# Kernel tuning notes

Measured on AMD Instinct MI355X. Metric: run time of the kernel, lower is better.

The kernel has to match this reference:

```python
import jax, jax.numpy as jnp
import numpy as np

NUM_HEADS = 16


def _rope(x_BHLd, freqs_cis):
    # x: [B,H,L,d], freqs_cis: [L, d//2, 2] (cos, sin)
    B, H, L, d = x_BHLd.shape
    xs = x_BHLd.reshape(B, H, L, d // 2, 2)
    fc = freqs_cis.reshape(1, 1, L, d // 2, 2)
    real = xs[..., 0] * fc[..., 0] - xs[..., 1] * fc[..., 1]
    imag = xs[..., 1] * fc[..., 0] + xs[..., 0] * fc[..., 1]
    return jnp.stack([real, imag], axis=-1).reshape(B, H, L, d)


def setup_inputs() -> dict:
    key = jax.random.key(0)
    k1, k2 = jax.random.split(key)
    B, L, D = 1, 4096, 1024
    d = D // NUM_HEADS
    x = jax.random.normal(k1, (B, L, D), dtype=jnp.float32)
    Wqkv = jax.random.normal(k2, (D, 3 * D), dtype=jnp.float32) * (D ** -0.5)
    bqkv = jnp.zeros((3 * D,), dtype=jnp.float32)
    # true rotary cos/sin table: [L, d//2, 2]
    base = 10000.0
    inv_freq = 1.0 / (base ** (jnp.arange(0, d, 2, dtype=jnp.float32) / d))  # [d//2]
    t = jnp.arange(L, dtype=jnp.float32)
    ang = jnp.outer(t, inv_freq)  # [L, d//2]
    freqs_cis = jnp.stack([jnp.cos(ang), jnp.sin(ang)], axis=-1)  # [L, d//2, 2]
    return {"x": x, "freqs_cis": freqs_cis, "Wqkv": Wqkv, "bqkv": bqkv}


def reference(x, freqs_cis, Wqkv, bqkv):
    B, L, D = x.shape
    H = NUM_HEADS
    d = D // H
    qkv = x @ Wqkv + bqkv  # [B,L,3D]
    q, k, v = jnp.split(qkv, 3, axis=-1)
    split = lambda t: t.reshape(B, L, H, d).transpose(0, 2, 1, 3)  # [B,H,L,d]
    q, k, v = split(q), split(k), split(v)
    q = _rope(q, freqs_cis)
    k = _rope(k, freqs_cis)
    scale = 1.0 / jnp.sqrt(jnp.asarray(d, dtype=q.dtype))
    scores = jnp.einsum('bhqd,bhkd->bhqk', q, k) * scale  # [B,H,L,L]
    causal = jnp.tril(jnp.ones((L, L), dtype=bool))
    scores = jnp.where(causal, scores, jnp.asarray(-jnp.inf, dtype=scores.dtype))
    probs = jax.nn.softmax(scores, axis=-1)
    out = jnp.einsum('bhqk,bhkd->bhqd', probs, v)  # [B,H,L,d]
    return out.transpose(0, 2, 1, 3).reshape(B, L, D)
```

## Files before the change

### kernel.cpp

```cpp
#include <hip/hip_runtime.h>

typedef short short8 __attribute__((ext_vector_type(8)));
typedef float f32x4 __attribute__((ext_vector_type(4)));
typedef unsigned short u16;
typedef unsigned short u16x4 __attribute__((ext_vector_type(4)));
typedef unsigned short u16x8 __attribute__((ext_vector_type(8)));

#define L_SEQ 4096
#define NHEAD 16
#define HDIM  64
#define DMODEL 1024
#define N3    3072
#define HL    (L_SEQ * HDIM)

__device__ __forceinline__ u16 f2bf(float f) {
  union { float f; unsigned u; } v; v.f = f;
  return (u16)((v.u + 0x7fffu + ((v.u >> 16) & 1u)) >> 16);
}

__device__ __forceinline__ unsigned cvt_pk_bf16(float lo, float hi) {
  unsigned r;
  asm("v_cvt_pk_bf16_f32 %0, %1, %2" : "=v"(r) : "v"(lo), "v"(hi));
  return r;
}

__device__ __forceinline__ void gl2lds16(const void* g, void* l) {
  __builtin_amdgcn_global_load_lds(
      (const __attribute__((address_space(1))) unsigned int*)g,
      (__attribute__((address_space(3))) unsigned int*)l, 16, 0, 0);
}

__device__ __forceinline__ float fexp2(float x) { return __builtin_amdgcn_exp2f(x); }

__global__ void cvt_fused_kernel(const float* __restrict__ x, u16* __restrict__ xb,
                                 const float* __restrict__ W, u16* __restrict__ Wt) {
  if (blockIdx.x < 2048) {
    int i = blockIdx.x * blockDim.x + threadIdx.x;
    const f32x4* p = (const f32x4*)x + (size_t)i * 2;
    f32x4 a = p[0], b = p[1];
    u16x8 o;
    o[0] = f2bf(a[0]); o[1] = f2bf(a[1]); o[2] = f2bf(a[2]); o[3] = f2bf(a[3]);
    o[4] = f2bf(b[0]); o[5] = f2bf(b[1]); o[6] = f2bf(b[2]); o[7] = f2bf(b[3]);
    ((u16x8*)xb)[i] = o;
  } else {
    __shared__ float t[64][65];
    int idx = blockIdx.x - 2048;
    int k0 = (idx & 15) * 64, n0 = (idx >> 4) * 64;
    int tr = threadIdx.x >> 4;
    int tc = (threadIdx.x & 15) * 4;
    for (int rr = tr; rr < 64; rr += 16) {
      f32x4 v = *(const f32x4*)&W[(size_t)(k0 + rr) * N3 + n0 + tc];
      t[rr][tc] = v[0]; t[rr][tc + 1] = v[1]; t[rr][tc + 2] = v[2]; t[rr][tc + 3] = v[3];
    }
    __syncthreads();
    for (int rr = tr; rr < 64; rr += 16) {
      u16x4 o;
      o[0] = f2bf(t[tc + 0][rr]); o[1] = f2bf(t[tc + 1][rr]);
      o[2] = f2bf(t[tc + 2][rr]); o[3] = f2bf(t[tc + 3][rr]);
      *(u16x4*)&Wt[(size_t)(n0 + rr) * DMODEL + k0 + tc] = o;
    }
  }
}

#define GBM 128
#define GBN 128
#define GBK 64

__global__ __launch_bounds__(256, 2) void gemm_qkv_kernel(
    const u16* __restrict__ xb, const u16* __restrict__ wt,
    const float* __restrict__ bias, const float* __restrict__ freqs,
    u16* __restrict__ Qb, u16* __restrict__ Kb, u16* __restrict__ Vt) {
  __shared__ u16 Asm[GBM * GBK];
  __shared__ u16 Bsm[GBN * GBK];
  const int tid = threadIdx.x, lane = tid & 63, wid = tid >> 6;
  const int lr = lane & 15, lh = lane >> 4;
  const int swz = (blockIdx.x % 8) * 96 + blockIdx.x / 8;
  const int bx = swz % (N3 / GBN), by = swz / (N3 / GBN);
  const int m0 = by * GBM, n0 = bx * GBN;
  const int wr = wid >> 1, wc = wid & 1;
  const char* xbB = (const char*)xb;
  const char* wtB = (const char*)wt;
  char* AsmB = (char*)Asm;
  char* BsmB = (char*)Bsm;

  int pbase[4]; size_t srcAoff[4], srcBoff[4];
#pragma unroll
  for (int i = 0; i < 4; i++) {
    int p = wid * 4096 + i * 1024 + lane * 16;
    int row = p >> 7, slot = (p & 127) >> 4;
    int sw = (slot ^ (row & 7)) * 16;
    pbase[i] = p;
    srcAoff[i] = (size_t)(m0 + row) * (DMODEL * 2) + sw;
    srcBoff[i] = (size_t)(n0 + row) * (DMODEL * 2) + sw;
  }

  int aoff[4][2], boff[4][2];
#pragma unroll
  for (int mi = 0; mi < 4; mi++) {
    int row = wr * 64 + mi * 16 + lr;
#pragma unroll
    for (int kc = 0; kc < 2; kc++)
      aoff[mi][kc] = row * 128 + ((kc * 64 + lh * 16) ^ ((row & 7) << 4));
  }
#pragma unroll
  for (int ni = 0; ni < 4; ni++) {
    int row = wc * 64 + ni * 16 + lr;
#pragma unroll
    for (int kc = 0; kc < 2; kc++)
      boff[ni][kc] = row * 128 + ((kc * 64 + lh * 16) ^ ((row & 7) << 4));
  }

  f32x4 acc[4][4] = {};

  for (int k0 = 0; k0 < DMODEL; k0 += GBK) {
    __syncthreads();
#pragma unroll
    for (int i = 0; i < 4; i++) {
      gl2lds16(xbB + srcAoff[i] + (size_t)k0 * 2, AsmB + pbase[i]);
      gl2lds16(wtB + srcBoff[i] + (size_t)k0 * 2, BsmB + pbase[i]);
    }
    __syncthreads();
#pragma unroll
    for (int kc = 0; kc < 2; kc++) {
      short8 a[4], b[4];
#pragma unroll
      for (int mi = 0; mi < 4; mi++) a[mi] = *(const short8*)(AsmB + aoff[mi][kc]);
#pragma unroll
      for (int ni = 0; ni < 4; ni++) b[ni] = *(const short8*)(BsmB + boff[ni][kc]);
#pragma unroll
      for (int mi = 0; mi < 4; mi++)
#pragma unroll
        for (int ni = 0; ni < 4; ni++)
          acc[mi][ni] = __builtin_amdgcn_mfma_f32_16x16x32_bf16(a[mi], b[ni], acc[mi][ni], 0, 0, 0);
    }
  }

  const float QSCALE = 0.125f * 1.44269504088896f;
  const int colbase = n0 + wc * 64;
#pragma unroll
  for (int ni = 0; ni < 4; ni++) {
    int col = colbase + ni * 16 + lr;
    float bv = bias[col];
    int sect = col >> 10;
    int cc = col & 1023;
    int h = cc >> 6, j = cc & 63;
#pragma unroll
    for (int mi = 0; mi < 4; mi++) {
      int row0 = m0 + wr * 64 + mi * 16 + lh * 4;
      float v[4];
#pragma unroll
      for (int r = 0; r < 4; r++) v[r] = acc[mi][ni][r] + bv;
      if (sect < 2) {
        int i2 = j >> 1;
        bool odd = (j & 1) != 0;
#pragma unroll
        for (int r = 0; r < 4; r++) {
          float pv = __shfl_xor(v[r], 1);
          float2 cs = *(const float2*)&freqs[((size_t)(row0 + r) * 32 + i2) * 2];
          v[r] = odd ? (v[r] * cs.x + pv * cs.y) : (v[r] * cs.x - pv * cs.y);
          if (sect == 0) v[r] *= QSCALE;
        }
        u16* dst = (sect == 0 ? Qb : Kb) + (size_t)h * HL + (size_t)row0 * HDIM + j;
#pragma unroll
        for (int r = 0; r < 4; r++) dst[(size_t)r * HDIM] = f2bf(v[r]);
      } else {
        u16x4 o;
#pragma unroll
        for (int r = 0; r < 4; r++) o[r] = f2bf(v[r]);
        *(u16x4*)&Vt[(size_t)h * HL + (size_t)j * L_SEQ + row0] = o;
      }
    }
  }
}

#define QBLK 64
#define KBLK 64

__global__ __launch_bounds__(256, 4) void flash_kernel(
    const u16* __restrict__ Qb, const u16* __restrict__ Kb,
    const u16* __restrict__ Vt, float* __restrict__ out) {
  __shared__ char Ksm[2][KBLK * 128];
  __shared__ char Vsm[2][HDIM * KBLK * 2];
  __shared__ char Psm[4][16 * 128];
  const int tid = threadIdx.x, lane = tid & 63, wid = tid >> 6;
  const int lr = lane & 15, lh = lane >> 4;
  const int bid = blockIdx.x;
  const int h = bid & 15;
  const int pr = bid >> 4;
  const char* Qh = (const char*)(Qb + (size_t)h * HL);
  const char* Kh = (const char*)(Kb + (size_t)h * HL);
  const char* Vh = (const char*)(Vt + (size_t)h * HL);
  char* Pw = Psm[wid];

  int pOff[2], KsrcOff[2], VsrcOff[2];
#pragma unroll
  for (int i = 0; i < 2; i++) {
    int p = wid * 2048 + i * 1024 + lane * 16;
    int row = p >> 7, slot = (p & 127) >> 4;
    int sw = (slot ^ (row & 7)) << 4;
    pOff[i] = p;
    KsrcOff[i] = row * 128 + sw;
    VsrcOff[i] = row * (L_SEQ * 2) + sw;
  }

  for (int pass = 0; pass < 2; ++pass) {
    const int qb = pass == 0 ? (63 - pr) : pr;
    const int q0 = qb * QBLK;
    const int wmin = q0 + wid * 16;
    const int qrow = wmin + lr;
    const int nt = qb + 1;

    short8 qa[2];
    {
      int row = q0 + wid * 16 + lr;
#pragma unroll
      for (int kc = 0; kc < 2; kc++)
        qa[kc] = *(const short8*)(Qh + (size_t)row * 128 + kc * 64 + lh * 16);
    }

    f32x4 o[4] = {};
    float m_r = -__builtin_inff(), ls = 0.f;

#pragma unroll
    for (int i = 0; i < 2; i++) {
      gl2lds16(Kh + KsrcOff[i], Ksm[0] + pOff[i]);
      gl2lds16(Vh + VsrcOff[i], Vsm[0] + pOff[i]);
    }
    __syncthreads();

    for (int t = 0; t < nt; ++t) {
      const int kt = t * KBLK;
      const int cur = t & 1;
      if (t + 1 < nt) {
        const size_t kn128 = (size_t)(kt + KBLK) * 128;
        const size_t kn2 = (size_t)(kt + KBLK) * 2;
#pragma unroll
        for (int i = 0; i < 2; i++) {
          gl2lds16(Kh + kn128 + KsrcOff[i], Ksm[cur ^ 1] + pOff[i]);
          gl2lds16(Vh + kn2 + VsrcOff[i], Vsm[cur ^ 1] + pOff[i]);
        }
      }
      const char* Kc = Ksm[cur];
      const char* Vc = Vsm[cur];

      f32x4 sfr[4];
      __builtin_amdgcn_s_setprio(1);
#pragma unroll
      for (int ni = 0; ni < 4; ni++) {
        int row = ni * 16 + lr;
        short8 bk0 = *(const short8*)(Kc + row * 128 + ((lh * 16) ^ ((row & 7) << 4)));
        short8 bk1 = *(const short8*)(Kc + row * 128 + ((64 + lh * 16) ^ ((row & 7) << 4)));
        f32x4 z = {};
        z = __builtin_amdgcn_mfma_f32_16x16x32_bf16(bk0, qa[0], z, 0, 0, 0);
        z = __builtin_amdgcn_mfma_f32_16x16x32_bf16(bk1, qa[1], z, 0, 0, 0);
        sfr[ni] = z;
      }
      __builtin_amdgcn_s_setprio(0);

      if (kt + KBLK - 1 > wmin) {
#pragma unroll
        for (int ni = 0; ni < 4; ni++)
#pragma unroll
          for (int r = 0; r < 4; r++)
            if (kt + ni * 16 + lh * 4 + r > qrow) sfr[ni][r] = -__builtin_inff();
      }

      float pmax = sfr[0][0];
#pragma unroll
      for (int ni = 0; ni < 4; ni++)
#pragma unroll
        for (int r = 0; r < 4; r++) pmax = fmaxf(pmax, sfr[ni][r]);
      pmax = fmaxf(pmax, __shfl_xor(pmax, 16));
      pmax = fmaxf(pmax, __shfl_xor(pmax, 32));

      if (__any(pmax > m_r + 8.f)) {
        float mn = fmaxf(m_r, pmax);
        float alpha = fexp2(m_r - mn);
        m_r = mn;
        ls *= alpha;
        float ao[4];
#pragma unroll
        for (int r = 0; r < 4; r++) ao[r] = __shfl(alpha, (lane & 48) | (lh * 4 + r));
#pragma unroll
        for (int vn = 0; vn < 4; vn++)
#pragma unroll
          for (int r = 0; r < 4; r++) o[vn][r] *= ao[r];
      }

      float psum = 0.f;
      unsigned Wp[4][2];
#pragma unroll
      for (int ni = 0; ni < 4; ni++) {
        float p0 = fexp2(sfr[ni][0] - m_r);
        float p1 = fexp2(sfr[ni][1] - m_r);
        float p2 = fexp2(sfr[ni][2] - m_r);
        float p3 = fexp2(sfr[ni][3] - m_r);
        psum += (p0 + p1) + (p2 + p3);
        Wp[ni][0] = cvt_pk_bf16(p0, p1);
        Wp[ni][1] = cvt_pk_bf16(p2, p3);
      }
      ls += psum;

#pragma unroll
      for (int ni = 0; ni < 4; ni++) {
        uint2 w2; w2.x = Wp[ni][0]; w2.y = Wp[ni][1];
        *(uint2*)(Pw + lr * 128 + ((ni * 32 + lh * 8) ^ ((lr & 7) << 4))) = w2;
      }
      asm volatile("s_waitcnt lgkmcnt(0)" ::: "memory");

      __builtin_amdgcn_s_setprio(1);
#pragma unroll
      for (int pc = 0; pc < 2; pc++) {
        short8 pa = *(const short8*)(Pw + lr * 128 + ((pc * 64 + lh * 16) ^ ((lr & 7) << 4)));
#pragma unroll
        for (int vn = 0; vn < 4; vn++) {
          int vrow = vn * 16 + lr;
          short8 bv = *(const short8*)(Vc + vrow * 128 + ((pc * 64 + lh * 16) ^ ((vrow & 7) << 4)));
          o[vn] = __builtin_amdgcn_mfma_f32_16x16x32_bf16(pa, bv, o[vn], 0, 0, 0);
        }
      }
      __builtin_amdgcn_s_setprio(0);

      __syncthreads();
    }

    ls += __shfl_xor(ls, 16);
    ls += __shfl_xor(ls, 32);
    float inv = 1.0f / ls;
    float invo[4];
#pragma unroll
    for (int r = 0; r < 4; r++) invo[r] = __shfl(inv, (lane & 48) | (lh * 4 + r));
#pragma unroll
    for (int r = 0; r < 4; r++) {
      int rowv = wmin + lh * 4 + r;
      float* op = out + (size_t)rowv * DMODEL + h * HDIM;
#pragma unroll
      for (int vn = 0; vn < 4; vn++) op[vn * 16 + lr] = o[vn][r] * invo[r];
    }
  }
}

extern "C" void kernel_launch(void* const* d_in, const int* in_sizes, int n_in,
                              void* d_out, int out_size, void* d_ws, size_t ws_size,
                              hipStream_t stream) {
  const float* x = (const float*)d_in[0];
  const float* freqs = (const float*)d_in[1];
  const float* W = (const float*)d_in[2];
  const float* bias = (const float*)d_in[3];
  float* out = (float*)d_out;

  char* ws = (char*)d_ws;
  u16* xb = (u16*)ws;
  u16* wt = (u16*)(ws + 8u * 1024 * 1024);
  u16* Qb = (u16*)(ws + 14u * 1024 * 1024);
  u16* Kb = (u16*)(ws + 22u * 1024 * 1024);
  u16* Vt = (u16*)(ws + 30u * 1024 * 1024);

  cvt_fused_kernel<<<2816, 256, 0, stream>>>(x, xb, W, wt);
  gemm_qkv_kernel<<<768, 256, 0, stream>>>(xb, wt, bias, freqs, Qb, Kb, Vt);
  flash_kernel<<<512, 256, 0, stream>>>(Qb, Kb, Vt, out);
}
```

Measured before the change: 129.4 us.

## Load V tiles directly from global into registers instead of via LDS

```diff
diff --git a/kernel.cpp b/kernel.cpp
--- a/kernel.cpp
+++ b/kernel.cpp
@@ -175,12 +175,12 @@
 
 #define QBLK 64
 #define KBLK 64
+#define LD8(p) (*(const short8*)(p))
 
 __global__ __launch_bounds__(256, 4) void flash_kernel(
     const u16* __restrict__ Qb, const u16* __restrict__ Kb,
     const u16* __restrict__ Vt, float* __restrict__ out) {
   __shared__ char Ksm[2][KBLK * 128];
-  __shared__ char Vsm[2][HDIM * KBLK * 2];
   __shared__ char Psm[4][16 * 128];
   const int tid = threadIdx.x, lane = tid & 63, wid = tid >> 6;
   const int lr = lane & 15, lh = lane >> 4;
@@ -192,16 +192,16 @@
   const char* Vh = (const char*)(Vt + (size_t)h * HL);
   char* Pw = Psm[wid];
 
-  int pOff[2], KsrcOff[2], VsrcOff[2];
+  int pOff[2], KsrcOff[2];
 #pragma unroll
   for (int i = 0; i < 2; i++) {
     int p = wid * 2048 + i * 1024 + lane * 16;
     int row = p >> 7, slot = (p & 127) >> 4;
-    int sw = (slot ^ (row & 7)) << 4;
     pOff[i] = p;
-    KsrcOff[i] = row * 128 + sw;
-    VsrcOff[i] = row * (L_SEQ * 2) + sw;
-  }
+    KsrcOff[i] = row * 128 + ((slot ^ (row & 7)) << 4);
+  }
+
+  const size_t vbase = (size_t)lr * (L_SEQ * 2) + (size_t)lh * 16;
 
   for (int pass = 0; pass < 2; ++pass) {
     const int qb = pass == 0 ? (63 - pr) : pr;
@@ -211,45 +211,41 @@
     const int nt = qb + 1;
 
     short8 qa[2];
-    {
-      int row = q0 + wid * 16 + lr;
-#pragma unroll
-      for (int kc = 0; kc < 2; kc++)
-        qa[kc] = *(const short8*)(Qh + (size_t)row * 128 + kc * 64 + lh * 16);
-    }
+#pragma unroll
+    for (int kc = 0; kc < 2; kc++)
+      qa[kc] = LD8(Qh + (size_t)qrow * 128 + kc * 64 + lh * 16);
 
     f32x4 o[4] = {};
     float m_r = -__builtin_inff(), ls = 0.f;
 
 #pragma unroll
-    for (int i = 0; i < 2; i++) {
+    for (int i = 0; i < 2; i++)
       gl2lds16(Kh + KsrcOff[i], Ksm[0] + pOff[i]);
-      gl2lds16(Vh + VsrcOff[i], Vsm[0] + pOff[i]);
-    }
+    short8 bv[4][2];
+#pragma unroll
+    for (int vn = 0; vn < 4; vn++)
+#pragma unroll
+      for (int pc = 0; pc < 2; pc++)
+        bv[vn][pc] = LD8(Vh + vbase + (size_t)vn * 16 * (L_SEQ * 2) + (size_t)pc * 64);
     __syncthreads();
 
     for (int t = 0; t < nt; ++t) {
       const int kt = t * KBLK;
       const int cur = t & 1;
       if (t + 1 < nt) {
-        const size_t kn128 = (size_t)(kt + KBLK) * 128;
-        const size_t kn2 = (size_t)(kt + KBLK) * 2;
-#pragma unroll
-        for (int i = 0; i < 2; i++) {
-          gl2lds16(Kh + kn128 + KsrcOff[i], Ksm[cur ^ 1] + pOff[i]);
-          gl2lds16(Vh + kn2 + VsrcOff[i], Vsm[cur ^ 1] + pOff[i]);
-        }
+#pragma unroll
+        for (int i = 0; i < 2; i++)
+          gl2lds16(Kh + (size_t)(kt + KBLK) * 128 + KsrcOff[i], Ksm[cur ^ 1] + pOff[i]);
       }
       const char* Kc = Ksm[cur];
-      const char* Vc = Vsm[cur];
 
       f32x4 sfr[4];
       __builtin_amdgcn_s_setprio(1);
 #pragma unroll
       for (int ni = 0; ni < 4; ni++) {
         int row = ni * 16 + lr;
-        short8 bk0 = *(const short8*)(Kc + row * 128 + ((lh * 16) ^ ((row & 7) << 4)));
-        short8 bk1 = *(const short8*)(Kc + row * 128 + ((64 + lh * 16) ^ ((row & 7) << 4)));
+        short8 bk0 = LD8(Kc + row * 128 + ((lh * 16) ^ ((row & 7) << 4)));
+        short8 bk1 = LD8(Kc + row * 128 + ((64 + lh * 16) ^ ((row & 7) << 4)));
         f32x4 z = {};
         z = __builtin_amdgcn_mfma_f32_16x16x32_bf16(bk0, qa[0], z, 0, 0, 0);
         z = __builtin_amdgcn_mfma_f32_16x16x32_bf16(bk1, qa[1], z, 0, 0, 0);
@@ -311,15 +307,21 @@
       __builtin_amdgcn_s_setprio(1);
 #pragma unroll
       for (int pc = 0; pc < 2; pc++) {
-        short8 pa = *(const short8*)(Pw + lr * 128 + ((pc * 64 + lh * 16) ^ ((lr & 7) << 4)));
-#pragma unroll
-        for (int vn = 0; vn < 4; vn++) {
-          int vrow = vn * 16 + lr;
-          short8 bv = *(const short8*)(Vc + vrow * 128 + ((pc * 64 + lh * 16) ^ ((vrow & 7) << 4)));
-          o[vn] = __builtin_amdgcn_mfma_f32_16x16x32_bf16(pa, bv, o[vn], 0, 0, 0);
-        }
+        short8 pa = LD8(Pw + lr * 128 + ((pc * 64 + lh * 16) ^ ((lr & 7) << 4)));
+#pragma unroll
+        for (int vn = 0; vn < 4; vn++)
+          o[vn] = __builtin_amdgcn_mfma_f32_16x16x32_bf16(pa, bv[vn][pc], o[vn], 0, 0, 0);
       }
       __builtin_amdgcn_s_setprio(0);
+
+      if (t + 1 < nt) {
+        const size_t kn2 = (size_t)(kt + KBLK) * 2;
+#pragma unroll
+        for (int vn = 0; vn < 4; vn++)
+#pragma unroll
+          for (int pc = 0; pc < 2; pc++)
+            bv[vn][pc] = LD8(Vh + vbase + (size_t)vn * 16 * (L_SEQ * 2) + kn2 + (size_t)pc * 64);
+      }
 
       __syncthreads();
     }
```

Result: slower. 182.0 us (+40.7%).
